# Optimization experiments

Measured on AMD Instinct MI355X. Metric: run time of the kernel, lower is better.

Reference implementation:

```python
import jax, jax.numpy as jnp
import numpy as np
from jax import lax

B, T = 8192, 128
HID = 64


def setup_inputs() -> dict:
    key = jax.random.key(0)
    ks = jax.random.split(key, 16)
    actor_ids = jax.random.randint(ks[0], (B, T), 0, 7, dtype=jnp.int32)
    action_ids = jax.random.randint(ks[1], (B, T), 0, 4, dtype=jnp.int32)
    street_ids = jax.random.randint(ks[2], (B, T), 0, 5, dtype=jnp.int32)
    bet_fraction = jax.random.uniform(ks[3], (B, T, 1), dtype=jnp.float32)
    # prefix-valid mask from random lengths (some zero-length rows)
    lengths = jax.random.randint(ks[4], (B,), 0, T + 1)
    valid_mask = jnp.arange(T)[None, :] < lengths[:, None]  # [B,T] bool
    s = 0.1
    params = {
        "E_actor": jax.random.normal(ks[5], (7, 8), jnp.float32) * s,
        "E_action": jax.random.normal(ks[6], (4, 8), jnp.float32) * s,
        "E_street": jax.random.normal(ks[7], (5, 4), jnp.float32) * s,
        "W_proj": jax.random.normal(ks[8], (32, 21), jnp.float32) * s,
        "b_proj": jax.random.normal(ks[9], (32,), jnp.float32) * s,
        "W_ih": jax.random.normal(ks[10], (3 * HID, 32), jnp.float32) * s,
        "W_hh": jax.random.normal(ks[11], (3 * HID, HID), jnp.float32) * s,
        "b_ih": jax.random.normal(ks[12], (3 * HID,), jnp.float32) * s,
        "b_hh": jax.random.normal(ks[13], (3 * HID,), jnp.float32) * s,
    }
    return dict(actor_ids=actor_ids, action_ids=action_ids, street_ids=street_ids,
                bet_fraction=bet_fraction, valid_mask=valid_mask, **params)


def reference(actor_ids, action_ids, street_ids, bet_fraction, valid_mask,
              E_actor, E_action, E_street, W_proj, b_proj,
              W_ih, W_hh, b_ih, b_hh):
    # embed + concat -> [B,T,21]
    feats = jnp.concatenate([E_actor[actor_ids], E_action[action_ids],
                             E_street[street_ids], bet_fraction], axis=-1)
    x = feats @ W_proj.T + b_proj                      # [B,T,32]
    # precompute input-side GRU gates for all timesteps: [B,T,3H]
    xg = x @ W_ih.T + b_ih
    xg_t = jnp.swapaxes(xg, 0, 1)                      # [T,B,3H]
    m_t = jnp.swapaxes(valid_mask, 0, 1)               # [T,B]

    def step(h, inp):
        xg_i, m = inp
        hg = h @ W_hh.T + b_hh                         # [B,3H]
        xr, xz, xn = jnp.split(xg_i, 3, axis=-1)
        hr, hz, hn = jnp.split(hg, 3, axis=-1)
        r = jax.nn.sigmoid(xr + hr)
        z = jax.nn.sigmoid(xz + hz)
        n = jnp.tanh(xn + r * hn)
        h_new = (1.0 - z) * n + z * h
        # only advance hidden state while t < length (prefix-valid mask);
        # final carry equals the GRU hidden at the last valid step, and rows
        # with length 0 stay at the zero init (matches torch masking).
        h = jnp.where(m[:, None], h_new, h)
        return h, None

    h0 = jnp.zeros((x.shape[0], HID), dtype=x.dtype)
    h_final, _ = lax.scan(step, h0, (xg_t, m_t))
    return h_final
```

## Files before the change

### kernel.cpp

```cpp
#include <hip/hip_runtime.h>

#define HID 64
#define TT  128
#define NROWS 8192
#define NGRP (NROWS / 16)
#define LOG2E 1.44269504088896f

typedef _Float16 half8 __attribute__((ext_vector_type(8)));
typedef float    f32x4 __attribute__((ext_vector_type(4)));

#define WS_WF    0
#define WS_WHH   12288
#define WS_BA    36864
#define WS_BX    37376
#define WS_BH    37632
#define WS_EMB   37888

__global__ __launch_bounds__(256) void prep(
    const float* __restrict__ E_actor, const float* __restrict__ E_action,
    const float* __restrict__ E_street, const float* __restrict__ W_proj,
    const float* __restrict__ b_proj, const float* __restrict__ W_ih,
    const float* __restrict__ b_ih, const float* __restrict__ W_hh,
    const float* __restrict__ b_hh, char* __restrict__ ws)
{
    _Float16* WF  = (_Float16*)(ws + WS_WF);
    _Float16* WHH = (_Float16*)(ws + WS_WHH);
    float*    BA  = (float*)(ws + WS_BA);
    float*    BX  = (float*)(ws + WS_BX);
    float*    BH  = (float*)(ws + WS_BH);
    _Float16* EMB = (_Float16*)(ws + WS_EMB);

    __shared__ float wfs[192][32];
    const int j = threadIdx.x;
    if (j < 192) {
        float wf[21];
        #pragma unroll
        for (int m = 0; m < 21; m++) wf[m] = 0.f;
        float bf = b_ih[j];
        for (int k = 0; k < 32; k++) {
            float w = W_ih[j * 32 + k];
            bf += w * b_proj[k];
            #pragma unroll
            for (int m = 0; m < 21; m++) wf[m] += w * W_proj[k * 21 + m];
        }
        const float s = (j < 128) ? LOG2E : 2.f * LOG2E;
        #pragma unroll
        for (int m = 0; m < 21; m++) wfs[j][m] = wf[m] * s;
        #pragma unroll
        for (int m = 21; m < 32; m++) wfs[j][m] = 0.f;
        if (j < 128) BA[j] = (bf + b_hh[j]) * LOG2E;
        else { BX[j - 128] = bf * 2.f * LOG2E; BH[j - 128] = b_hh[j] * 2.f * LOG2E; }
    }
    if (j < 17 * 8) {
        int r = j >> 3, m = j & 7;
        float v = 0.f;
        if (r < 7)       v = E_actor[r * 8 + m];
        else if (r < 11) v = E_action[(r - 7) * 8 + m];
        else if (r < 16) v = (m < 4) ? E_street[(r - 11) * 4 + m] : 0.f;
        EMB[j] = (_Float16)v;
    }
    __syncthreads();

    for (int idx = j; idx < 12 * 64; idx += 256) {
        const int T = idx >> 6, lane = idx & 63;
        const int g3 = T >> 2, w = T & 3, m16 = lane & 15, kq = lane >> 4;
        const int jr = g3 * 64 + w * 16 + m16;
        _Float16 v[8];
        #pragma unroll
        for (int m = 0; m < 8; m++) v[m] = (_Float16)wfs[jr][kq * 8 + m];
        *(uint4*)&WF[idx * 8] = *(uint4*)v;
    }
    for (int idx = j; idx < 12 * 2 * 64; idx += 256) {
        const int T = idx >> 7, rem = idx & 127, kt = rem >> 6, lane = rem & 63;
        const int g3 = T >> 2, w = T & 3, m16 = lane & 15, kq = lane >> 4;
        const int jr = g3 * 64 + w * 16 + m16;
        const int kbase = kt * 32 + kq * 8;
        const float s = (jr < 128) ? LOG2E : 2.f * LOG2E;
        _Float16 v[8];
        #pragma unroll
        for (int m = 0; m < 8; m++) v[m] = (_Float16)(W_hh[jr * HID + kbase + m] * s);
        *(uint4*)&WHH[((T * 2 + kt) * 64 + lane) * 8] = *(uint4*)v;
    }
}

__global__ __launch_bounds__(256, 2) void gru_mfma(
    const int* __restrict__ actor_ids, const int* __restrict__ action_ids,
    const int* __restrict__ street_ids, const float* __restrict__ bet,
    const int* __restrict__ mask, const char* __restrict__ ws,
    float* __restrict__ out)
{
    const _Float16* WF  = (const _Float16*)(ws + WS_WF);
    const _Float16* WHH = (const _Float16*)(ws + WS_WHH);
    const float*    BA  = (const float*)(ws + WS_BA);
    const float*    BX  = (const float*)(ws + WS_BX);
    const float*    BH  = (const float*)(ws + WS_BH);
    const _Float16* EMB = (const _Float16*)(ws + WS_EMB);

    __shared__ int pb[TT][17];
    __shared__ __align__(16) _Float16 hb[2][16][72];
    __shared__ __align__(16) _Float16 embl[144];
    __shared__ int part[16][16];
    __shared__ int Lsh[16];

    const int tid = threadIdx.x;
    const int wv  = tid >> 6;
    const int l   = tid & 63;
    const int q   = l >> 4;
    const int n   = l & 15;

    const int g = blockIdx.x;

    for (int i = tid; i < 136; i += 256) embl[i] = EMB[i];
    for (int i = tid; i < 2 * 16 * 72 / 2; i += 256) ((int*)hb)[i] = 0;
    {
        const int r = tid >> 4, tl = tid & 15;
        const int base = (g * 16 + r) * TT;
        int cnt = 0;
        #pragma unroll
        for (int i = 0; i < 8; i++) {
            const int t = tl + 16 * i;
            const int a = actor_ids[base + t], c = action_ids[base + t];
            const int s = street_ids[base + t];
            const _Float16 f16 = (_Float16)bet[base + t];
            const unsigned fb = (unsigned)*(const unsigned short*)&f16;
            pb[t][r] = (int)(a | (c << 3) | (s << 5) | (fb << 16));
            cnt += (mask[base + t] != 0);
        }
        part[r][tl] = cnt;
    }

    half8 Af[3], Ah[3][2];
    #pragma unroll
    for (int g3 = 0; g3 < 3; g3++) {
        const int T = g3 * 4 + wv;
        Af[g3]    = *(const half8*)&WF[(T * 64 + l) * 8];
        Ah[g3][0] = *(const half8*)&WHH[((T * 2 + 0) * 64 + l) * 8];
        Ah[g3][1] = *(const half8*)&WHH[((T * 2 + 1) * 64 + l) * 8];
    }
    f32x4 biasR, biasZ, biasX, biasH;
    #pragma unroll
    for (int e = 0; e < 4; e++) {
        const int idx = 16 * wv + 4 * q + e;
        biasR[e] = BA[idx];
        biasZ[e] = BA[64 + idx];
        biasX[e] = BX[idx];
        biasH[e] = BH[idx];
    }

    __syncthreads();
    if (tid < 16) {
        int L = 0;
        #pragma unroll
        for (int i = 0; i < 16; i++) L += part[tid][i];
        Lsh[tid] = L;
    }
    __syncthreads();

    const int Ln = Lsh[n];
    int Lmax = Ln;
    #pragma unroll
    for (int k = 1; k < 16; k <<= 1) {
        const int o = __shfl_xor(Lmax, k);
        Lmax = (o > Lmax) ? o : Lmax;
    }

    const bool isq2 = (q == 2);
    float h[4] = {0.f, 0.f, 0.f, 0.f};
    const f32x4 zero4 = {0.f, 0.f, 0.f, 0.f};

    f32x4 xR, xZ, xX;
    {
        const int p = pb[0][n];
        const int a = p & 7, c = (p >> 3) & 3, s = (p >> 5) & 7;
        const int eidx = (q == 0) ? a : (q == 1) ? (7 + c) : isq2 ? (11 + s) : 16;
        half8 Bf = *(const half8*)&embl[eidx * 8];
        uint4* bu = (uint4*)&Bf;
        bu->z = isq2 ? ((unsigned)p >> 16) : bu->z;
        xR = __builtin_amdgcn_mfma_f32_16x16x32_f16(Af[0], Bf, biasR, 0, 0, 0);
        xZ = __builtin_amdgcn_mfma_f32_16x16x32_f16(Af[1], Bf, biasZ, 0, 0, 0);
        xX = __builtin_amdgcn_mfma_f32_16x16x32_f16(Af[2], Bf, biasX, 0, 0, 0);
    }

    for (int t = 0; t < Lmax; t++) {
        const int buf = t & 1;
        const half8 Bh0 = *(const half8*)&hb[buf][n][q * 8];
        const half8 Bh1 = *(const half8*)&hb[buf][n][32 + q * 8];
        f32x4 aR0 = __builtin_amdgcn_mfma_f32_16x16x32_f16(Ah[0][0], Bh0, xR, 0, 0, 0);
        f32x4 aR1 = __builtin_amdgcn_mfma_f32_16x16x32_f16(Ah[0][1], Bh1, zero4, 0, 0, 0);
        f32x4 aZ0 = __builtin_amdgcn_mfma_f32_16x16x32_f16(Ah[1][0], Bh0, xZ, 0, 0, 0);
        f32x4 aZ1 = __builtin_amdgcn_mfma_f32_16x16x32_f16(Ah[1][1], Bh1, zero4, 0, 0, 0);
        f32x4 aH0 = __builtin_amdgcn_mfma_f32_16x16x32_f16(Ah[2][0], Bh0, biasH, 0, 0, 0);
        f32x4 aH1 = __builtin_amdgcn_mfma_f32_16x16x32_f16(Ah[2][1], Bh1, zero4, 0, 0, 0);
        const f32x4 aXc = xX;

        {
            const int tn = (t + 1 < TT) ? t + 1 : TT - 1;
            const int p = pb[tn][n];
            const int a = p & 7, c = (p >> 3) & 3, s = (p >> 5) & 7;
            const int eidx = (q == 0) ? a : (q == 1) ? (7 + c) : isq2 ? (11 + s) : 16;
            half8 Bf = *(const half8*)&embl[eidx * 8];
            uint4* bu = (uint4*)&Bf;
            bu->z = isq2 ? ((unsigned)p >> 16) : bu->z;
            xR = __builtin_amdgcn_mfma_f32_16x16x32_f16(Af[0], Bf, biasR, 0, 0, 0);
            xZ = __builtin_amdgcn_mfma_f32_16x16x32_f16(Af[1], Bf, biasZ, 0, 0, 0);
            xX = __builtin_amdgcn_mfma_f32_16x16x32_f16(Af[2], Bf, biasX, 0, 0, 0);
        }

        const f32x4 aR = aR0 + aR1, aZ = aZ0 + aZ1, aH = aH0 + aH1;
        const bool live = (t < Ln);
        _Float16 hp[4];
        #pragma unroll
        for (int e = 0; e < 4; e++) {
            const float r = __builtin_amdgcn_rcpf(1.f + __builtin_amdgcn_exp2f(-aR[e]));
            const float z = __builtin_amdgcn_rcpf(1.f + __builtin_amdgcn_exp2f(-aZ[e]));
            const float y2 = aXc[e] + r * aH[e];
            const float nn = 1.f - 2.f * __builtin_amdgcn_rcpf(1.f + __builtin_amdgcn_exp2f(y2));
            const float hv = nn + z * (h[e] - nn);
            h[e] = live ? hv : h[e];
            hp[e] = (_Float16)h[e];
        }
        *(uint2*)&hb[buf ^ 1][n][16 * wv + 4 * q] = *(uint2*)hp;
        __syncthreads();
    }

    float4 o = make_float4(h[0], h[1], h[2], h[3]);
    *(float4*)&out[(g * 16 + n) * HID + 16 * wv + 4 * q] = o;
}

extern "C" void kernel_launch(void* const* d_in, const int* in_sizes, int n_in,
                              void* d_out, int out_size, void* d_ws, size_t ws_size,
                              hipStream_t stream) {
    const int*   actor_ids  = (const int*)d_in[0];
    const int*   action_ids = (const int*)d_in[1];
    const int*   street_ids = (const int*)d_in[2];
    const float* bet        = (const float*)d_in[3];
    const int*   vmask      = (const int*)d_in[4];
    const float* E_actor    = (const float*)d_in[5];
    const float* E_action   = (const float*)d_in[6];
    const float* E_street   = (const float*)d_in[7];
    const float* W_proj     = (const float*)d_in[8];
    const float* b_proj     = (const float*)d_in[9];
    const float* W_ih       = (const float*)d_in[10];
    const float* W_hh       = (const float*)d_in[11];
    const float* b_ih       = (const float*)d_in[12];
    const float* b_hh       = (const float*)d_in[13];
    float*       out        = (float*)d_out;

    char* ws = (char*)d_ws;
    prep<<<1, 256, 0, stream>>>(E_actor, E_action, E_street, W_proj, b_proj,
                                W_ih, b_ih, W_hh, b_hh, ws);
    gru_mfma<<<NGRP, 256, 0, stream>>>(actor_ids, action_ids, street_ids, bet,
                                       vmask, ws, out);
}
```

Baseline: 169.8 us.

## Fuse weight-prep kernel into GRU kernel and chain MFMA accumulations

```diff
diff --git a/kernel.cpp b/kernel.cpp
--- a/kernel.cpp
+++ b/kernel.cpp
@@ -9,109 +9,98 @@
 typedef _Float16 half8 __attribute__((ext_vector_type(8)));
 typedef float    f32x4 __attribute__((ext_vector_type(4)));
 
-#define WS_WF    0
-#define WS_WHH   12288
-#define WS_BA    36864
-#define WS_BX    37376
-#define WS_BH    37632
-#define WS_EMB   37888
-
-__global__ __launch_bounds__(256) void prep(
+__global__ __launch_bounds__(256, 2) void gru_fused(
+    const int* __restrict__ actor_ids, const int* __restrict__ action_ids,
+    const int* __restrict__ street_ids, const float* __restrict__ bet,
+    const int* __restrict__ mask,
     const float* __restrict__ E_actor, const float* __restrict__ E_action,
     const float* __restrict__ E_street, const float* __restrict__ W_proj,
     const float* __restrict__ b_proj, const float* __restrict__ W_ih,
     const float* __restrict__ b_ih, const float* __restrict__ W_hh,
-    const float* __restrict__ b_hh, char* __restrict__ ws)
+    const float* __restrict__ b_hh, float* __restrict__ out)
 {
-    _Float16* WF  = (_Float16*)(ws + WS_WF);
-    _Float16* WHH = (_Float16*)(ws + WS_WHH);
-    float*    BA  = (float*)(ws + WS_BA);
-    float*    BX  = (float*)(ws + WS_BX);
-    float*    BH  = (float*)(ws + WS_BH);
-    _Float16* EMB = (_Float16*)(ws + WS_EMB);
-
-    __shared__ float wfs[192][32];
-    const int j = threadIdx.x;
-    if (j < 192) {
-        float wf[21];
-        #pragma unroll
-        for (int m = 0; m < 21; m++) wf[m] = 0.f;
-        float bf = b_ih[j];
-        for (int k = 0; k < 32; k++) {
-            float w = W_ih[j * 32 + k];
-            bf += w * b_proj[k];
-            #pragma unroll
-            for (int m = 0; m < 21; m++) wf[m] += w * W_proj[k * 21 + m];
-        }
-        const float s = (j < 128) ? LOG2E : 2.f * LOG2E;
-        #pragma unroll
-        for (int m = 0; m < 21; m++) wfs[j][m] = wf[m] * s;
-        #pragma unroll
-        for (int m = 21; m < 32; m++) wfs[j][m] = 0.f;
-        if (j < 128) BA[j] = (bf + b_hh[j]) * LOG2E;
-        else { BX[j - 128] = bf * 2.f * LOG2E; BH[j - 128] = b_hh[j] * 2.f * LOG2E; }
-    }
-    if (j < 17 * 8) {
-        int r = j >> 3, m = j & 7;
-        float v = 0.f;
-        if (r < 7)       v = E_actor[r * 8 + m];
-        else if (r < 11) v = E_action[(r - 7) * 8 + m];
-        else if (r < 16) v = (m < 4) ? E_street[(r - 11) * 4 + m] : 0.f;
-        EMB[j] = (_Float16)v;
-    }
-    __syncthreads();
-
-    for (int idx = j; idx < 12 * 64; idx += 256) {
-        const int T = idx >> 6, lane = idx & 63;
-        const int g3 = T >> 2, w = T & 3, m16 = lane & 15, kq = lane >> 4;
-        const int jr = g3 * 64 + w * 16 + m16;
-        _Float16 v[8];
-        #pragma unroll
-        for (int m = 0; m < 8; m++) v[m] = (_Float16)wfs[jr][kq * 8 + m];
-        *(uint4*)&WF[idx * 8] = *(uint4*)v;
-    }
-    for (int idx = j; idx < 12 * 2 * 64; idx += 256) {
-        const int T = idx >> 7, rem = idx & 127, kt = rem >> 6, lane = rem & 63;
-        const int g3 = T >> 2, w = T & 3, m16 = lane & 15, kq = lane >> 4;
-        const int jr = g3 * 64 + w * 16 + m16;
-        const int kbase = kt * 32 + kq * 8;
-        const float s = (jr < 128) ? LOG2E : 2.f * LOG2E;
-        _Float16 v[8];
-        #pragma unroll
-        for (int m = 0; m < 8; m++) v[m] = (_Float16)(W_hh[jr * HID + kbase + m] * s);
-        *(uint4*)&WHH[((T * 2 + kt) * 64 + lane) * 8] = *(uint4*)v;
-    }
-}
-
-__global__ __launch_bounds__(256, 2) void gru_mfma(
-    const int* __restrict__ actor_ids, const int* __restrict__ action_ids,
-    const int* __restrict__ street_ids, const float* __restrict__ bet,
-    const int* __restrict__ mask, const char* __restrict__ ws,
-    float* __restrict__ out)
-{
-    const _Float16* WF  = (const _Float16*)(ws + WS_WF);
-    const _Float16* WHH = (const _Float16*)(ws + WS_WHH);
-    const float*    BA  = (const float*)(ws + WS_BA);
-    const float*    BX  = (const float*)(ws + WS_BX);
-    const float*    BH  = (const float*)(ws + WS_BH);
-    const _Float16* EMB = (const _Float16*)(ws + WS_EMB);
-
-    __shared__ int pb[TT][17];
-    __shared__ __align__(16) _Float16 hb[2][16][72];
+    __shared__ __align__(16) union {
+        float wfs[192][32];
+        struct {
+            int pb[TT][17];
+            __align__(16) _Float16 hb[2][16][72];
+            int part[16][16];
+            int Lsh[16];
+        } c;
+    } A;
     __shared__ __align__(16) _Float16 embl[144];
-    __shared__ int part[16][16];
-    __shared__ int Lsh[16];
+    __shared__ float bfs[192];
 
     const int tid = threadIdx.x;
     const int wv  = tid >> 6;
     const int l   = tid & 63;
     const int q   = l >> 4;
     const int n   = l & 15;
-
-    const int g = blockIdx.x;
-
-    for (int i = tid; i < 136; i += 256) embl[i] = EMB[i];
-    for (int i = tid; i < 2 * 16 * 72 / 2; i += 256) ((int*)hb)[i] = 0;
+    const int g   = blockIdx.x;
+
+    for (int i = tid; i < 136; i += 256) {
+        int r = i >> 3, m = i & 7;
+        float v = 0.f;
+        if (r < 7)       v = E_actor[r * 8 + m];
+        else if (r < 11) v = E_action[(r - 7) * 8 + m];
+        else if (r < 16) v = (m < 4) ? E_street[(r - 11) * 4 + m] : 0.f;
+        embl[i] = (_Float16)v;
+    }
+
+    if (tid < 192) {
+        const int j = tid;
+        float wf[21];
+        #pragma unroll
+        for (int m = 0; m < 21; m++) wf[m] = 0.f;
+        float bf = b_ih[j];
+        for (int k = 0; k < 32; k++) {
+            const float w = W_ih[j * 32 + k];
+            bf += w * b_proj[k];
+            #pragma unroll
+            for (int m = 0; m < 21; m++) wf[m] += w * W_proj[k * 21 + m];
+        }
+        const float s = (j < 128) ? LOG2E : 2.f * LOG2E;
+        #pragma unroll
+        for (int m = 0; m < 21; m++) A.wfs[j][m] = wf[m] * s;
+        #pragma unroll
+        for (int m = 21; m < 32; m++) A.wfs[j][m] = 0.f;
+        bfs[j] = bf;
+    }
+    __syncthreads();
+
+    half8 Af[3], Ah[3][2];
+    {
+        const int m16 = l & 15, kq = l >> 4;
+        #pragma unroll
+        for (int g3 = 0; g3 < 3; g3++) {
+            const int jr = g3 * 64 + wv * 16 + m16;
+            _Float16 v[8];
+            #pragma unroll
+            for (int m = 0; m < 8; m++) v[m] = (_Float16)A.wfs[jr][kq * 8 + m];
+            Af[g3] = *(half8*)v;
+            const float s = (g3 < 2) ? LOG2E : 2.f * LOG2E;
+            #pragma unroll
+            for (int kt = 0; kt < 2; kt++) {
+                _Float16 w[8];
+                #pragma unroll
+                for (int m = 0; m < 8; m++)
+                    w[m] = (_Float16)(W_hh[jr * HID + kt * 32 + kq * 8 + m] * s);
+                Ah[g3][kt] = *(half8*)w;
+            }
+        }
+    }
+    f32x4 biasR, biasZ, biasX, biasH;
+    #pragma unroll
+    for (int e = 0; e < 4; e++) {
+        const int idx = 16 * wv + 4 * q + e;
+        biasR[e] = (bfs[idx]      + b_hh[idx])      * LOG2E;
+        biasZ[e] = (bfs[64 + idx] + b_hh[64 + idx]) * LOG2E;
+        biasX[e] = bfs[128 + idx]  * (2.f * LOG2E);
+        biasH[e] = b_hh[128 + idx] * (2.f * LOG2E);
+    }
+    __syncthreads();
+
+    for (int i = tid; i < 2 * 16 * 72 / 2; i += 256) ((int*)A.c.hb)[i] = 0;
     {
         const int r = tid >> 4, tl = tid & 15;
         const int base = (g * 16 + r) * TT;
@@ -123,40 +112,21 @@
             const int s = street_ids[base + t];
             const _Float16 f16 = (_Float16)bet[base + t];
             const unsigned fb = (unsigned)*(const unsigned short*)&f16;
-            pb[t][r] = (int)(a | (c << 3) | (s << 5) | (fb << 16));
+            A.c.pb[t][r] = (int)(a | (c << 3) | (s << 5) | (fb << 16));
             cnt += (mask[base + t] != 0);
         }
-        part[r][tl] = cnt;
-    }
-
-    half8 Af[3], Ah[3][2];
-    #pragma unroll
-    for (int g3 = 0; g3 < 3; g3++) {
-        const int T = g3 * 4 + wv;
-        Af[g3]    = *(const half8*)&WF[(T * 64 + l) * 8];
-        Ah[g3][0] = *(const half8*)&WHH[((T * 2 + 0) * 64 + l) * 8];
-        Ah[g3][1] = *(const half8*)&WHH[((T * 2 + 1) * 64 + l) * 8];
-    }
-    f32x4 biasR, biasZ, biasX, biasH;
-    #pragma unroll
-    for (int e = 0; e < 4; e++) {
-        const int idx = 16 * wv + 4 * q + e;
-        biasR[e] = BA[idx];
-        biasZ[e] = BA[64 + idx];
-        biasX[e] = BX[idx];
-        biasH[e] = BH[idx];
-    }
-
+        A.c.part[r][tl] = cnt;
+    }
     __syncthreads();
     if (tid < 16) {
         int L = 0;
         #pragma unroll
-        for (int i = 0; i < 16; i++) L += part[tid][i];
-        Lsh[tid] = L;
-    }
-    __syncthreads();
-
-    const int Ln = Lsh[n];
+        for (int i = 0; i < 16; i++) L += A.c.part[tid][i];
+        A.c.Lsh[tid] = L;
+    }
+    __syncthreads();
+
+    const int Ln = A.c.Lsh[n];
     int Lmax = Ln;
     #pragma unroll
     for (int k = 1; k < 16; k <<= 1) {
@@ -165,14 +135,16 @@
     }
 
     const bool isq2 = (q == 2);
+    const int sh = (q == 1) ? 3 : (q == 2) ? 5 : 0;
+    const int mk = (q == 1) ? 3 : (q == 3) ? 0 : 7;
+    const int of = (q == 1) ? 7 : (q == 2) ? 11 : (q == 3) ? 16 : 0;
+
     float h[4] = {0.f, 0.f, 0.f, 0.f};
-    const f32x4 zero4 = {0.f, 0.f, 0.f, 0.f};
 
     f32x4 xR, xZ, xX;
     {
-        const int p = pb[0][n];
-        const int a = p & 7, c = (p >> 3) & 3, s = (p >> 5) & 7;
-        const int eidx = (q == 0) ? a : (q == 1) ? (7 + c) : isq2 ? (11 + s) : 16;
+        const int p = A.c.pb[0][n];
+        const int eidx = ((p >> sh) & mk) + of;
         half8 Bf = *(const half8*)&embl[eidx * 8];
         uint4* bu = (uint4*)&Bf;
         bu->z = isq2 ? ((unsigned)p >> 16) : bu->z;
@@ -183,21 +155,20 @@
 
     for (int t = 0; t < Lmax; t++) {
         const int buf = t & 1;
-        const half8 Bh0 = *(const half8*)&hb[buf][n][q * 8];
-        const half8 Bh1 = *(const half8*)&hb[buf][n][32 + q * 8];
-        f32x4 aR0 = __builtin_amdgcn_mfma_f32_16x16x32_f16(Ah[0][0], Bh0, xR, 0, 0, 0);
-        f32x4 aR1 = __builtin_amdgcn_mfma_f32_16x16x32_f16(Ah[0][1], Bh1, zero4, 0, 0, 0);
-        f32x4 aZ0 = __builtin_amdgcn_mfma_f32_16x16x32_f16(Ah[1][0], Bh0, xZ, 0, 0, 0);
-        f32x4 aZ1 = __builtin_amdgcn_mfma_f32_16x16x32_f16(Ah[1][1], Bh1, zero4, 0, 0, 0);
-        f32x4 aH0 = __builtin_amdgcn_mfma_f32_16x16x32_f16(Ah[2][0], Bh0, biasH, 0, 0, 0);
-        f32x4 aH1 = __builtin_amdgcn_mfma_f32_16x16x32_f16(Ah[2][1], Bh1, zero4, 0, 0, 0);
+        const half8 Bh0 = *(const half8*)&A.c.hb[buf][n][q * 8];
+        const half8 Bh1 = *(const half8*)&A.c.hb[buf][n][32 + q * 8];
+        f32x4 aR = __builtin_amdgcn_mfma_f32_16x16x32_f16(Ah[0][0], Bh0, xR, 0, 0, 0);
+        aR = __builtin_amdgcn_mfma_f32_16x16x32_f16(Ah[0][1], Bh1, aR, 0, 0, 0);
+        f32x4 aZ = __builtin_amdgcn_mfma_f32_16x16x32_f16(Ah[1][0], Bh0, xZ, 0, 0, 0);
+        aZ = __builtin_amdgcn_mfma_f32_16x16x32_f16(Ah[1][1], Bh1, aZ, 0, 0, 0);
+        f32x4 aH = __builtin_amdgcn_mfma_f32_16x16x32_f16(Ah[2][0], Bh0, biasH, 0, 0, 0);
+        aH = __builtin_amdgcn_mfma_f32_16x16x32_f16(Ah[2][1], Bh1, aH, 0, 0, 0);
         const f32x4 aXc = xX;
 
         {
             const int tn = (t + 1 < TT) ? t + 1 : TT - 1;
-            const int p = pb[tn][n];
-            const int a = p & 7, c = (p >> 3) & 3, s = (p >> 5) & 7;
-            const int eidx = (q == 0) ? a : (q == 1) ? (7 + c) : isq2 ? (11 + s) : 16;
+            const int p = A.c.pb[tn][n];
+            const int eidx = ((p >> sh) & mk) + of;
             half8 Bf = *(const half8*)&embl[eidx * 8];
             uint4* bu = (uint4*)&Bf;
             bu->z = isq2 ? ((unsigned)p >> 16) : bu->z;
@@ -206,7 +177,6 @@
             xX = __builtin_amdgcn_mfma_f32_16x16x32_f16(Af[2], Bf, biasX, 0, 0, 0);
         }
 
-        const f32x4 aR = aR0 + aR1, aZ = aZ0 + aZ1, aH = aH0 + aH1;
         const bool live = (t < Ln);
         _Float16 hp[4];
         #pragma unroll
@@ -219,7 +189,7 @@
             h[e] = live ? hv : h[e];
             hp[e] = (_Float16)h[e];
         }
-        *(uint2*)&hb[buf ^ 1][n][16 * wv + 4 * q] = *(uint2*)hp;
+        *(uint2*)&A.c.hb[buf ^ 1][n][16 * wv + 4 * q] = *(uint2*)hp;
         __syncthreads();
     }
 
@@ -246,9 +216,8 @@
     const float* b_hh       = (const float*)d_in[13];
     float*       out        = (float*)d_out;
 
-    char* ws = (char*)d_ws;
-    prep<<<1, 256, 0, stream>>>(E_actor, E_action, E_street, W_proj, b_proj,
-                                W_ih, b_ih, W_hh, b_hh, ws);
-    gru_mfma<<<NGRP, 256, 0, stream>>>(actor_ids, action_ids, street_ids, bet,
-                                       vmask, ws, out);
+    gru_fused<<<NGRP, 256, 0, stream>>>(actor_ids, action_ids, street_ids, bet,
+                                        vmask, E_actor, E_action, E_street,
+                                        W_proj, b_proj, W_ih, b_ih, W_hh, b_hh,
+                                        out);
 }
```

Result: faster. 166.0 us (median of 2 runs) (-2.2%).
